# Kernel tuning notes

Measured on AMD Instinct MI355X. Metric: run time of the kernel, lower is better.

Reference implementation:

```python
import jax, jax.numpy as jnp
import numpy as np

B, D, H, W = 32, 256, 32, 32
K = 1024
COMMITMENT_COST = 0.25


def setup_inputs() -> dict:
    key = jax.random.key(0)
    k1, k2 = jax.random.split(key)
    z = jax.random.normal(k1, (B, D, H, W), dtype=jnp.float32)
    # torch init: uniform_(-1/K, 1/K)
    emb_weight = jax.random.uniform(k2, (K, D), dtype=jnp.float32,
                                    minval=-1.0 / K, maxval=1.0 / K)
    return {"z": z, "emb_weight": emb_weight}


def reference(z, emb_weight):
    b, c, h, w = z.shape
    # [B, D, H, W] -> [B*H*W, D]
    z_flat = jnp.transpose(z, (0, 2, 3, 1)).reshape(-1, c)
    # squared-distance: ||z||^2 + ||e||^2 - 2 z.e  -> [N, K]
    distances = (jnp.sum(z_flat ** 2, axis=1, keepdims=True)
                 + jnp.sum(emb_weight ** 2, axis=1)[None, :]
                 - 2.0 * jnp.matmul(z_flat, emb_weight.T))
    encoding_indices = jnp.argmin(distances, axis=1)  # [N]
    z_q = emb_weight[encoding_indices]                # [N, D]
    z_q = z_q.reshape(b, h, w, c).transpose(0, 3, 1, 2)  # [B, D, H, W]

    q_latent_loss = jnp.mean((jax.lax.stop_gradient(z_q) - z) ** 2)
    e_latent_loss = jnp.mean((z_q - jax.lax.stop_gradient(z)) ** 2)
    loss = q_latent_loss + COMMITMENT_COST * e_latent_loss

    # straight-through estimator
    z_q = z + jax.lax.stop_gradient(z_q - z)
    return z_q, loss, encoding_indices
```

## Files before the change

kernel.cpp:

```cpp
#include <hip/hip_runtime.h>

#define NPTS  32768
#define DIM   256
#define KCB   1024

#define ZQ_OFF   0
#define LOSS_OFF 8388608
#define IDX_OFF  8388609

typedef __attribute__((ext_vector_type(8))) short short8;
typedef __attribute__((ext_vector_type(4))) float f32x4;

__device__ __forceinline__ int z_base(int n) { return ((n >> 10) << 18) | (n & 1023); }

__device__ __forceinline__ unsigned short f2bf(float f) {
    unsigned u = __float_as_uint(f);
    u += 0x7FFFu + ((u >> 16) & 1u);
    return (unsigned short)(u >> 16);
}

__device__ __forceinline__ unsigned long long pack_vi(float v, int i) {
    unsigned int u = __float_as_uint(v);
    unsigned int key = (u & 0x80000000u) ? ~u : u;
    return ((unsigned long long)key << 32) | (unsigned int)i;
}

__device__ __forceinline__ float np_half_sq(const float* __restrict__ p, int stride) {
    float S[16];
#pragma unroll
    for (int l = 0; l < 16; ++l) {
        float t[8];
#pragma unroll
        for (int j = 0; j < 8; ++j) {
            float v = p[(j * 16 + l) * stride];
            t[j] = __fmul_rn(v, v);
        }
        S[l] = __fadd_rn(__fadd_rn(__fadd_rn(t[0], t[1]), __fadd_rn(t[2], t[3])),
                         __fadd_rn(__fadd_rn(t[4], t[5]), __fadd_rn(t[6], t[7])));
    }
    float u[8];
#pragma unroll
    for (int i = 0; i < 8; ++i) u[i] = __fadd_rn(S[i], S[i + 8]);
    float v4[4];
#pragma unroll
    for (int i = 0; i < 4; ++i) v4[i] = __fadd_rn(u[i], u[i + 4]);
    return __fadd_rn(__fadd_rn(v4[0], v4[2]), __fadd_rn(v4[1], v4[3]));
}
__device__ __forceinline__ float np_sum256_sq(const float* __restrict__ p, int stride) {
    return __fadd_rn(np_half_sq(p, stride), np_half_sq(p + 128 * stride, stride));
}

__global__ __launch_bounds__(256) void setup_kernel(
    const float* __restrict__ z, const float* __restrict__ emb,
    float* __restrict__ z2, float* __restrict__ eps,
    float* __restrict__ e2, float* __restrict__ e2h,
    unsigned short* __restrict__ ebf,
    double* __restrict__ loss_acc, unsigned int* __restrict__ ticket)
{
    if (blockIdx.x < 128) {
        int n = blockIdx.x * 256 + threadIdx.x;
        const float* p = z + z_base(n);
        z2[n] = np_sum256_sq(p, 1024);
        float a = 0.0f;
#pragma unroll 8
        for (int d = 0; d < 256; ++d) a += fabsf(p[d << 10]);
        eps[n] = __builtin_fmaf(1e-5f, a, 3e-4f);
        if (blockIdx.x == 0 && threadIdx.x == 0) { *loss_acc = 0.0; *ticket = 0u; }
    } else {
        int kb = (blockIdx.x - 128) * 256;
        for (int idx = threadIdx.x; idx < 256 * 256; idx += 256) {
            int k = kb + (idx >> 8), d = idx & 255;
            ebf[k * 256 + d] = f2bf(emb[k * 256 + d]);
        }
        int k = kb + threadIdx.x;
        float s = np_sum256_sq(emb + k * DIM, 1);
        e2[k] = s;
        e2h[k] = 0.5f * s;
    }
}

#define ZS_STRIDE 264
#define ES_STRIDE 40
#define ES_SIZE   (128 * ES_STRIDE)

__global__ __launch_bounds__(256) void dist_kernel(
    const float* __restrict__ z, const float* __restrict__ emb,
    const unsigned short* __restrict__ ebf,
    const float* __restrict__ z2w, const float* __restrict__ e2w,
    const float* __restrict__ e2hw, const float* __restrict__ epsw,
    float* __restrict__ out_idx)
{
    __shared__ __align__(16) short zs[64 * ZS_STRIDE];
    __shared__ __align__(16) short es[2 * ES_SIZE];
    __shared__ float redbuf[64 * 32];
    __shared__ int   cl[64 * 32];
    __shared__ float MxS[64], thrS[64], epsS[64], z2S[64];
    __shared__ unsigned int cntS[64];
    __shared__ unsigned long long bestS[64];
    __shared__ int ovfS;

    const int tid = threadIdx.x;
    const int w  = tid >> 6;
    const int l  = tid & 63;
    const int lq = l >> 4;
    const int lr = l & 15;
    const int n0 = blockIdx.x << 6;
    const int zb = z_base(n0);

    if (tid < 64) {
        MxS[tid] = -3.4e38f; thrS[tid] = 3.4e38f;
        cntS[tid] = 0u; bestS[tid] = 0x7FFFFFFFFFFFFFFFULL;
        epsS[tid] = epsw[n0 + tid]; z2S[tid] = z2w[n0 + tid];
    }
    if (tid == 0) ovfS = 0;
    for (int i = tid; i < 64 * 32; i += 256) cl[i] = 0;

    {
        int q = tid & 15, d0 = tid >> 4;
#pragma unroll 4
        for (int i = 0; i < 16; ++i) {
            int d = d0 + 16 * i;
            float4 v = *(const float4*)(z + zb + (d << 10) + 4 * q);
            zs[(4 * q + 0) * ZS_STRIDE + d] = (short)f2bf(v.x);
            zs[(4 * q + 1) * ZS_STRIDE + d] = (short)f2bf(v.y);
            zs[(4 * q + 2) * ZS_STRIDE + d] = (short)f2bf(v.z);
            zs[(4 * q + 3) * ZS_STRIDE + d] = (short)f2bf(v.w);
        }
    }

    const int skk = tid >> 1, sh = tid & 1;

    {
        const int4* src = (const int4*)(ebf + skk * 256 + sh * 16);
        int4 a = src[0], b = src[1];
        int4* dst = (int4*)(es + skk * ES_STRIDE + sh * 16);
        dst[0] = a; dst[1] = b;
    }
    __syncthreads();

    f32x4 acc[2][4];
#pragma unroll
    for (int mt = 0; mt < 2; ++mt)
#pragma unroll
        for (int nt = 0; nt < 4; ++nt) acc[mt][nt] = (f32x4)0.0f;

    const int mrow = 32 * (w & 1);
    const int kwv  = 64 * (w >> 1);

    int4 pa, pb;
#pragma unroll 1
    for (int g = 0; g < 72; ++g) {
        const int kt = g >> 3, dt = g & 7;
        const int k0 = (kt < 8 ? kt : 0) * 128;
        if (g < 71) {
            int gn = g + 1;
            int k0n = ((gn >> 3) < 8 ? (gn >> 3) : 0) * 128;
            const int4* src = (const int4*)(ebf + (k0n + skk) * 256 + (gn & 7) * 32 + sh * 16);
            pa = src[0]; pb = src[1];
        }
        {
            const short* esb = es + (g & 1) * ES_SIZE;
            const int dbase = dt * 32;
            short8 af0 = *(const short8*)(zs + (mrow + lr) * ZS_STRIDE + dbase + lq * 8);
            short8 af1 = *(const short8*)(zs + (mrow + 16 + lr) * ZS_STRIDE + dbase + lq * 8);
#pragma unroll
            for (int nt = 0; nt < 4; ++nt) {
                short8 bf = *(const short8*)(esb + (kwv + 16 * nt + lr) * ES_STRIDE + lq * 8);
                acc[0][nt] = __builtin_amdgcn_mfma_f32_16x16x32_bf16(af0, bf, acc[0][nt], 0, 0, 0);
                acc[1][nt] = __builtin_amdgcn_mfma_f32_16x16x32_bf16(af1, bf, acc[1][nt], 0, 0, 0);
            }
        }
        if (g < 71) {
            int4* dst = (int4*)(es + ((g + 1) & 1) * ES_SIZE + skk * ES_STRIDE + sh * 16);
            dst[0] = pa; dst[1] = pb;
            __syncthreads();
        }
        if (dt == 7) {
            if (g == 71) __syncthreads();
            float e2hr[4]; int kg[4];
#pragma unroll
            for (int nt = 0; nt < 4; ++nt) {
                kg[nt] = k0 + kwv + 16 * nt + lr;
                e2hr[nt] = e2hw[kg[nt]];
            }
            float vals[2][4][4];
#pragma unroll
            for (int mt = 0; mt < 2; ++mt)
#pragma unroll
                for (int nt = 0; nt < 4; ++nt)
#pragma unroll
                    for (int r = 0; r < 4; ++r)
                        vals[mt][nt][r] = acc[mt][nt][r] - e2hr[nt];
            if (kt < 8) {
#pragma unroll
                for (int mt = 0; mt < 2; ++mt)
#pragma unroll
                    for (int r = 0; r < 4; ++r) {
                        float m = fmaxf(fmaxf(vals[mt][0][r], vals[mt][1][r]),
                                        fmaxf(vals[mt][2][r], vals[mt][3][r]));
                        int row = mrow + 16 * mt + lq * 4 + r;
                        redbuf[row * 32 + (w >> 1) * 16 + lr] = m;
                    }
                __syncthreads();
                if (tid < 64) {
                    float m = redbuf[tid * 32];
#pragma unroll 8
                    for (int c = 1; c < 32; ++c) m = fmaxf(m, redbuf[tid * 32 + c]);
                    float Mx = fmaxf(MxS[tid], m);
                    MxS[tid] = Mx;
                    thrS[tid] = Mx - epsS[tid];
                }
                __syncthreads();
            }
            if (kt >= 1) {
#pragma unroll
                for (int mt = 0; mt < 2; ++mt)
#pragma unroll
                    for (int r = 0; r < 4; ++r) {
                        int row = mrow + 16 * mt + lq * 4 + r;
                        float th = thrS[row];
#pragma unroll
                        for (int nt = 0; nt < 4; ++nt) {
                            if (vals[mt][nt][r] >= th) {
                                unsigned int p = atomicAdd(&cntS[row], 1u);
                                if (p < 32u) cl[row * 32 + p] = kg[nt];
                                else atomicMax(&ovfS, 1);
                            }
                        }
                    }
            }
            if (kt < 8) {
#pragma unroll
                for (int mt = 0; mt < 2; ++mt)
#pragma unroll
                    for (int nt = 0; nt < 4; ++nt) acc[mt][nt] = (f32x4)0.0f;
            }
        }
    }

    __syncthreads();
    float* zx = (float*)es;
    const int pt = tid & 63;
    const int s0 = tid >> 6;
    unsigned int nc = cntS[pt]; if (nc > 32u) nc = 32u;
    bool  act[8]; int kE[8]; float accE[8];
#pragma unroll
    for (int j = 0; j < 8; ++j) {
        unsigned int s = (unsigned int)s0 + 4u * j;
        act[j] = s < nc;
        kE[j] = act[j] ? cl[pt * 32 + s] : 0;
        accE[j] = 0.0f;
    }
#pragma unroll 1
    for (int dt = 0; dt < 8; ++dt) {
        const int dbase = dt * 32;
        __syncthreads();
        {
            int q = tid & 15, dd0 = tid >> 4;
            float4 v0 = *(const float4*)(z + zb + ((dbase + dd0) << 10) + 4 * q);
            float4 v1 = *(const float4*)(z + zb + ((dbase + dd0 + 16) << 10) + 4 * q);
            *(float4*)(zx + dd0 * 68 + 4 * q) = v0;
            *(float4*)(zx + (dd0 + 16) * 68 + 4 * q) = v1;
        }
        __syncthreads();
#pragma unroll
        for (int j = 0; j < 8; ++j) {
            if (!act[j]) continue;
            const float* er = emb + kE[j] * 256 + dbase;
            float ev[32];
#pragma unroll
            for (int c = 0; c < 8; ++c) *(float4*)(ev + 4 * c) = *(const float4*)(er + 4 * c);
            float a = accE[j];
#pragma unroll
            for (int dd = 0; dd < 32; ++dd)
                a = __builtin_fmaf(zx[dd * 68 + pt], ev[dd], a);
            accE[j] = a;
        }
    }
#pragma unroll
    for (int j = 0; j < 8; ++j) {
        if (!act[j]) continue;
        int k = kE[j];
        float t1 = __fadd_rn(z2S[pt], e2w[k]);
        float d  = __fsub_rn(t1, __fmul_rn(2.0f, accE[j]));
        atomicMin(&bestS[pt], pack_vi(d, k));
    }
    __syncthreads();

    if (ovfS) {
        for (int row = 0; row < 64; ++row) {
            if (cntS[row] <= 32u) continue;
            float fa[4] = {0.f, 0.f, 0.f, 0.f};
            for (int dt = 0; dt < 8; ++dt) {
                const int dbase = dt * 32;
                __syncthreads();
                {
                    int q = tid & 15, dd0 = tid >> 4;
                    float4 v0 = *(const float4*)(z + zb + ((dbase + dd0) << 10) + 4 * q);
                    float4 v1 = *(const float4*)(z + zb + ((dbase + dd0 + 16) << 10) + 4 * q);
                    *(float4*)(zx + dd0 * 68 + 4 * q) = v0;
                    *(float4*)(zx + (dd0 + 16) * 68 + 4 * q) = v1;
                }
                __syncthreads();
                for (int c = 0; c < 4; ++c) {
                    const float* er = emb + (tid + 256 * c) * 256 + dbase;
                    for (int dd = 0; dd < 32; ++dd)
                        fa[c] = __builtin_fmaf(zx[dd * 68 + row], er[dd], fa[c]);
                }
            }
            for (int c = 0; c < 4; ++c) {
                int k = tid + 256 * c;
                float t1 = __fadd_rn(z2S[row], e2w[k]);
                float d  = __fsub_rn(t1, __fmul_rn(2.0f, fa[c]));
                atomicMin(&bestS[row], pack_vi(d, k));
            }
            __syncthreads();
        }
    }

    if (tid < 64)
        out_idx[n0 + tid] = (float)(unsigned int)(bestS[tid] & 0xFFFFFFFFULL);
}

__global__ __launch_bounds__(256) void zq_loss_kernel(
    const float* __restrict__ z, const float* __restrict__ emb,
    const float* __restrict__ idxv, float* __restrict__ zq,
    double* __restrict__ loss_acc, unsigned int* __restrict__ ticket,
    float* __restrict__ out_loss)
{
    const int n = blockIdx.x * 256 + threadIdx.x;
    const int kk = (int)idxv[n];
    const float* er = emb + kk * DIM;
    const int zb = z_base(n);
    double s = 0.0;
#pragma unroll 8
    for (int d = 0; d < DIM; ++d) {
        float ev = er[d];
        float zv = z[zb + (d << 10)];
        zq[zb + (d << 10)] = ev;
        float df = ev - zv;
        s = fma((double)df, (double)df, s);
    }
    for (int off = 32; off; off >>= 1) s += __shfl_down(s, off, 64);
    __shared__ double sred[4];
    if ((threadIdx.x & 63) == 0) sred[threadIdx.x >> 6] = s;
    __syncthreads();
    if (threadIdx.x == 0) {
        atomicAdd(loss_acc, (sred[0] + sred[1]) + (sred[2] + sred[3]));
        __threadfence();
        unsigned int old = atomicAdd(ticket, 1u);
        if (old == gridDim.x - 1) {
            double total = atomicAdd(loss_acc, 0.0);
            out_loss[0] = (float)(1.25 * (total / 8388608.0));
        }
    }
}

extern "C" void kernel_launch(void* const* d_in, const int* in_sizes, int n_in,
                              void* d_out, int out_size, void* d_ws, size_t ws_size,
                              hipStream_t stream) {
    const float* z   = (const float*)d_in[0];
    const float* emb = (const float*)d_in[1];
    float* out = (float*)d_out;

    float* z2w = (float*)d_ws;
    float* epsw = (float*)((char*)d_ws + 131072);
    float* e2w = (float*)((char*)d_ws + 262144);
    float* e2hw = (float*)((char*)d_ws + 266240);
    unsigned short* ebf = (unsigned short*)((char*)d_ws + 270336);
    double* loss_acc = (double*)((char*)d_ws + 794624);
    unsigned int* ticket = (unsigned int*)((char*)d_ws + 794632);

    setup_kernel<<<132, 256, 0, stream>>>(z, emb, z2w, epsw, e2w, e2hw, ebf,
                                          loss_acc, ticket);
    dist_kernel<<<NPTS / 64, 256, 0, stream>>>(z, emb, ebf, z2w, e2w, e2hw, epsw,
                                               out + IDX_OFF);
    zq_loss_kernel<<<NPTS / 256, 256, 0, stream>>>(z, emb, out + IDX_OFF,
                                                   out + ZQ_OFF, loss_acc, ticket,
                                                   out + LOSS_OFF);
}
```

Baseline: 250.2 us.

## Fuse zq/loss into distance kernel and stream codebook directly from global memory

The distance kernel is restructured so each wave owns a 256-entry slice of the codebook across all 64 points. It loads bf16 codebook fragments straight from global memory into registers and drops the LDS double buffer and the per-chunk block-wide syncs. Row maxima are reduced with cross-lane shuffles per wave instead of a shared redbuf and two barriers, and the candidate list grows to 48 slots. The zq gather and loss accumulation are fused into the tail of the same kernel, which removes the third launch, and setup fuses the abs-sum pass and vectorises the bf16 conversion. The risks are more global traffic for codebook fragments, more registers, and a per-wave running max that may be looser and admit more candidates.

Result: slower. 263.9 us (+5.5%).

```diff
diff --git a/kernel.cpp b/kernel.cpp
--- a/kernel.cpp
+++ b/kernel.cpp
@@ -44,6 +44,30 @@
     float v4[4];
 #pragma unroll
     for (int i = 0; i < 4; ++i) v4[i] = __fadd_rn(u[i], u[i + 4]);
+    return __fadd_rn(__fadd_rn(v4[0], v4[2]), __fadd_rn(v4[1], v4[3]));
+}
+__device__ __forceinline__ float np_half_sq_abs(const float* __restrict__ p, int stride,
+                                                float* asum) {
+    float S[16]; float a = *asum;
+#pragma unroll
+    for (int l = 0; l < 16; ++l) {
+        float t[8];
+#pragma unroll
+        for (int j = 0; j < 8; ++j) {
+            float v = p[(j * 16 + l) * stride];
+            t[j] = __fmul_rn(v, v);
+            a += fabsf(v);
+        }
+        S[l] = __fadd_rn(__fadd_rn(__fadd_rn(t[0], t[1]), __fadd_rn(t[2], t[3])),
+                         __fadd_rn(__fadd_rn(t[4], t[5]), __fadd_rn(t[6], t[7])));
+    }
+    float u[8];
+#pragma unroll
+    for (int i = 0; i < 8; ++i) u[i] = __fadd_rn(S[i], S[i + 8]);
+    float v4[4];
+#pragma unroll
+    for (int i = 0; i < 4; ++i) v4[i] = __fadd_rn(u[i], u[i + 4]);
+    *asum = a;
     return __fadd_rn(__fadd_rn(v4[0], v4[2]), __fadd_rn(v4[1], v4[3]));
 }
 __device__ __forceinline__ float np_sum256_sq(const float* __restrict__ p, int stride) {
@@ -60,17 +84,19 @@
     if (blockIdx.x < 128) {
         int n = blockIdx.x * 256 + threadIdx.x;
         const float* p = z + z_base(n);
-        z2[n] = np_sum256_sq(p, 1024);
         float a = 0.0f;
-#pragma unroll 8
-        for (int d = 0; d < 256; ++d) a += fabsf(p[d << 10]);
+        float h0 = np_half_sq_abs(p, 1024, &a);
+        float h1 = np_half_sq_abs(p + 128 * 1024, 1024, &a);
+        z2[n] = __fadd_rn(h0, h1);
         eps[n] = __builtin_fmaf(1e-5f, a, 3e-4f);
         if (blockIdx.x == 0 && threadIdx.x == 0) { *loss_acc = 0.0; *ticket = 0u; }
     } else {
         int kb = (blockIdx.x - 128) * 256;
-        for (int idx = threadIdx.x; idx < 256 * 256; idx += 256) {
-            int k = kb + (idx >> 8), d = idx & 255;
-            ebf[k * 256 + d] = f2bf(emb[k * 256 + d]);
+        const float2* s2 = (const float2*)(emb + kb * 256);
+        unsigned int* d2 = (unsigned int*)(ebf + kb * 256);
+        for (int i = threadIdx.x; i < 256 * 128; i += 256) {
+            float2 v = s2[i];
+            d2[i] = (unsigned)f2bf(v.x) | ((unsigned)f2bf(v.y) << 16);
         }
         int k = kb + threadIdx.x;
         float s = np_sum256_sq(emb + k * DIM, 1);
@@ -80,175 +106,158 @@
 }
 
 #define ZS_STRIDE 264
-#define ES_STRIDE 40
-#define ES_SIZE   (128 * ES_STRIDE)
-
-__global__ __launch_bounds__(256) void dist_kernel(
+#define CL_SLOTS  48
+
+__global__ __launch_bounds__(256) void dist_fused_kernel(
     const float* __restrict__ z, const float* __restrict__ emb,
     const unsigned short* __restrict__ ebf,
     const float* __restrict__ z2w, const float* __restrict__ e2w,
     const float* __restrict__ e2hw, const float* __restrict__ epsw,
-    float* __restrict__ out_idx)
+    float* __restrict__ out_idx, float* __restrict__ zq,
+    double* __restrict__ loss_acc, unsigned int* __restrict__ ticket,
+    float* __restrict__ out_loss)
 {
     __shared__ __align__(16) short zs[64 * ZS_STRIDE];
-    __shared__ __align__(16) short es[2 * ES_SIZE];
-    __shared__ float redbuf[64 * 32];
-    __shared__ int   cl[64 * 32];
-    __shared__ float MxS[64], thrS[64], epsS[64], z2S[64];
+    __shared__ int clS[64 * CL_SLOTS];
     __shared__ unsigned int cntS[64];
     __shared__ unsigned long long bestS[64];
+    __shared__ float z2S[64];
+    __shared__ double sredL[4];
     __shared__ int ovfS;
 
     const int tid = threadIdx.x;
-    const int w  = tid >> 6;
-    const int l  = tid & 63;
-    const int lq = l >> 4;
-    const int lr = l & 15;
-    const int n0 = blockIdx.x << 6;
-    const int zb = z_base(n0);
+    const int w   = tid >> 6;
+    const int l   = tid & 63;
+    const int n16 = l & 15;
+    const int q   = l >> 4;
+    const int n0  = blockIdx.x << 6;
+    const int zb  = z_base(n0);
+    const int kq  = w << 8;
 
     if (tid < 64) {
-        MxS[tid] = -3.4e38f; thrS[tid] = 3.4e38f;
-        cntS[tid] = 0u; bestS[tid] = 0x7FFFFFFFFFFFFFFFULL;
-        epsS[tid] = epsw[n0 + tid]; z2S[tid] = z2w[n0 + tid];
+        cntS[tid] = 0u;
+        bestS[tid] = 0x7FFFFFFFFFFFFFFFULL;
+        z2S[tid] = z2w[n0 + tid];
     }
     if (tid == 0) ovfS = 0;
-    for (int i = tid; i < 64 * 32; i += 256) cl[i] = 0;
 
     {
-        int q = tid & 15, d0 = tid >> 4;
+        int qq = tid & 15, d0 = tid >> 4;
 #pragma unroll 4
         for (int i = 0; i < 16; ++i) {
             int d = d0 + 16 * i;
-            float4 v = *(const float4*)(z + zb + (d << 10) + 4 * q);
-            zs[(4 * q + 0) * ZS_STRIDE + d] = (short)f2bf(v.x);
-            zs[(4 * q + 1) * ZS_STRIDE + d] = (short)f2bf(v.y);
-            zs[(4 * q + 2) * ZS_STRIDE + d] = (short)f2bf(v.z);
-            zs[(4 * q + 3) * ZS_STRIDE + d] = (short)f2bf(v.w);
-        }
-    }
-
-    const int skk = tid >> 1, sh = tid & 1;
-
-    {
-        const int4* src = (const int4*)(ebf + skk * 256 + sh * 16);
-        int4 a = src[0], b = src[1];
-        int4* dst = (int4*)(es + skk * ES_STRIDE + sh * 16);
-        dst[0] = a; dst[1] = b;
-    }
-    __syncthreads();
-
-    f32x4 acc[2][4];
-#pragma unroll
-    for (int mt = 0; mt < 2; ++mt)
+            float4 v = *(const float4*)(z + zb + (d << 10) + 4 * qq);
+            zs[(4 * qq + 0) * ZS_STRIDE + d] = (short)f2bf(v.x);
+            zs[(4 * qq + 1) * ZS_STRIDE + d] = (short)f2bf(v.y);
+            zs[(4 * qq + 2) * ZS_STRIDE + d] = (short)f2bf(v.z);
+            zs[(4 * qq + 3) * ZS_STRIDE + d] = (short)f2bf(v.w);
+        }
+    }
+
+    float epsr[4][4];
+#pragma unroll
+    for (int mt = 0; mt < 4; ++mt)
+#pragma unroll
+        for (int r = 0; r < 4; ++r)
+            epsr[mt][r] = epsw[n0 + mt * 16 + q * 4 + r];
+
+    __syncthreads();
+
+    f32x4 acc[4][4];
+    float Mx[4][4];
+#pragma unroll
+    for (int mt = 0; mt < 4; ++mt)
 #pragma unroll
         for (int nt = 0; nt < 4; ++nt) acc[mt][nt] = (f32x4)0.0f;
-
-    const int mrow = 32 * (w & 1);
-    const int kwv  = 64 * (w >> 1);
-
-    int4 pa, pb;
+#pragma unroll
+    for (int mt = 0; mt < 4; ++mt)
+#pragma unroll
+        for (int r = 0; r < 4; ++r) Mx[mt][r] = -3.4e38f;
+
+    int4 bcur[4];
+#pragma unroll
+    for (int nt = 0; nt < 4; ++nt)
+        bcur[nt] = *(const int4*)(ebf + ((kq + nt * 16 + n16) << 8) + q * 8);
+
 #pragma unroll 1
-    for (int g = 0; g < 72; ++g) {
-        const int kt = g >> 3, dt = g & 7;
-        const int k0 = (kt < 8 ? kt : 0) * 128;
-        if (g < 71) {
-            int gn = g + 1;
-            int k0n = ((gn >> 3) < 8 ? (gn >> 3) : 0) * 128;
-            const int4* src = (const int4*)(ebf + (k0n + skk) * 256 + (gn & 7) * 32 + sh * 16);
-            pa = src[0]; pb = src[1];
-        }
-        {
-            const short* esb = es + (g & 1) * ES_SIZE;
-            const int dbase = dt * 32;
-            short8 af0 = *(const short8*)(zs + (mrow + lr) * ZS_STRIDE + dbase + lq * 8);
-            short8 af1 = *(const short8*)(zs + (mrow + 16 + lr) * ZS_STRIDE + dbase + lq * 8);
+    for (int step = 0; step < 32; ++step) {
+        const int s = step >> 3, dc = step & 7;
+        short8 af[4];
+#pragma unroll
+        for (int mt = 0; mt < 4; ++mt)
+            af[mt] = *(const short8*)(zs + (mt * 16 + n16) * ZS_STRIDE + dc * 32 + q * 8);
+#pragma unroll
+        for (int nt = 0; nt < 4; ++nt) {
+            short8 bf = *(short8*)&bcur[nt];
+#pragma unroll
+            for (int mt = 0; mt < 4; ++mt)
+                acc[mt][nt] = __builtin_amdgcn_mfma_f32_16x16x32_bf16(af[mt], bf, acc[mt][nt], 0, 0, 0);
+        }
+        if (step < 31) {
+            const int sn = (step + 1) >> 3, dcn = (step + 1) & 7;
+#pragma unroll
+            for (int nt = 0; nt < 4; ++nt)
+                bcur[nt] = *(const int4*)(ebf + ((kq + sn * 64 + nt * 16 + n16) << 8) + dcn * 32 + q * 8);
+        }
+        if (dc == 7) {
+            float e2hr[4]; int kg[4];
 #pragma unroll
             for (int nt = 0; nt < 4; ++nt) {
-                short8 bf = *(const short8*)(esb + (kwv + 16 * nt + lr) * ES_STRIDE + lq * 8);
-                acc[0][nt] = __builtin_amdgcn_mfma_f32_16x16x32_bf16(af0, bf, acc[0][nt], 0, 0, 0);
-                acc[1][nt] = __builtin_amdgcn_mfma_f32_16x16x32_bf16(af1, bf, acc[1][nt], 0, 0, 0);
-            }
-        }
-        if (g < 71) {
-            int4* dst = (int4*)(es + ((g + 1) & 1) * ES_SIZE + skk * ES_STRIDE + sh * 16);
-            dst[0] = pa; dst[1] = pb;
-            __syncthreads();
-        }
-        if (dt == 7) {
-            if (g == 71) __syncthreads();
-            float e2hr[4]; int kg[4];
-#pragma unroll
-            for (int nt = 0; nt < 4; ++nt) {
-                kg[nt] = k0 + kwv + 16 * nt + lr;
+                kg[nt] = kq + s * 64 + nt * 16 + n16;
                 e2hr[nt] = e2hw[kg[nt]];
             }
-            float vals[2][4][4];
-#pragma unroll
-            for (int mt = 0; mt < 2; ++mt)
+#pragma unroll
+            for (int mt = 0; mt < 4; ++mt)
 #pragma unroll
                 for (int nt = 0; nt < 4; ++nt)
 #pragma unroll
                     for (int r = 0; r < 4; ++r)
-                        vals[mt][nt][r] = acc[mt][nt][r] - e2hr[nt];
-            if (kt < 8) {
-#pragma unroll
-                for (int mt = 0; mt < 2; ++mt)
-#pragma unroll
-                    for (int r = 0; r < 4; ++r) {
-                        float m = fmaxf(fmaxf(vals[mt][0][r], vals[mt][1][r]),
-                                        fmaxf(vals[mt][2][r], vals[mt][3][r]));
-                        int row = mrow + 16 * mt + lq * 4 + r;
-                        redbuf[row * 32 + (w >> 1) * 16 + lr] = m;
-                    }
-                __syncthreads();
-                if (tid < 64) {
-                    float m = redbuf[tid * 32];
-#pragma unroll 8
-                    for (int c = 1; c < 32; ++c) m = fmaxf(m, redbuf[tid * 32 + c]);
-                    float Mx = fmaxf(MxS[tid], m);
-                    MxS[tid] = Mx;
-                    thrS[tid] = Mx - epsS[tid];
+                        acc[mt][nt][r] -= e2hr[nt];
+#pragma unroll
+            for (int mt = 0; mt < 4; ++mt)
+#pragma unroll
+                for (int r = 0; r < 4; ++r) {
+                    float m = fmaxf(fmaxf(acc[mt][0][r], acc[mt][1][r]),
+                                    fmaxf(acc[mt][2][r], acc[mt][3][r]));
+                    m = fmaxf(m, __shfl_xor(m, 1, 64));
+                    m = fmaxf(m, __shfl_xor(m, 2, 64));
+                    m = fmaxf(m, __shfl_xor(m, 4, 64));
+                    m = fmaxf(m, __shfl_xor(m, 8, 64));
+                    Mx[mt][r] = fmaxf(Mx[mt][r], m);
                 }
-                __syncthreads();
-            }
-            if (kt >= 1) {
-#pragma unroll
-                for (int mt = 0; mt < 2; ++mt)
-#pragma unroll
-                    for (int r = 0; r < 4; ++r) {
-                        int row = mrow + 16 * mt + lq * 4 + r;
-                        float th = thrS[row];
-#pragma unroll
-                        for (int nt = 0; nt < 4; ++nt) {
-                            if (vals[mt][nt][r] >= th) {
-                                unsigned int p = atomicAdd(&cntS[row], 1u);
-                                if (p < 32u) cl[row * 32 + p] = kg[nt];
-                                else atomicMax(&ovfS, 1);
-                            }
+#pragma unroll
+            for (int mt = 0; mt < 4; ++mt)
+#pragma unroll
+                for (int r = 0; r < 4; ++r) {
+                    const float th = Mx[mt][r] - epsr[mt][r];
+                    const int row = mt * 16 + q * 4 + r;
+#pragma unroll
+                    for (int nt = 0; nt < 4; ++nt) {
+                        if (acc[mt][nt][r] >= th) {
+                            unsigned int p = atomicAdd(&cntS[row], 1u);
+                            if (p < CL_SLOTS) clS[row * CL_SLOTS + p] = kg[nt];
+                            else ovfS = 1;
                         }
                     }
-            }
-            if (kt < 8) {
-#pragma unroll
-                for (int mt = 0; mt < 2; ++mt)
-#pragma unroll
-                    for (int nt = 0; nt < 4; ++nt) acc[mt][nt] = (f32x4)0.0f;
-            }
-        }
-    }
-
-    __syncthreads();
-    float* zx = (float*)es;
+                }
+#pragma unroll
+            for (int mt = 0; mt < 4; ++mt)
+#pragma unroll
+                for (int nt = 0; nt < 4; ++nt) acc[mt][nt] = (f32x4)0.0f;
+        }
+    }
+
+    __syncthreads();
+    float* zx = (float*)zs;
     const int pt = tid & 63;
     const int s0 = tid >> 6;
-    unsigned int nc = cntS[pt]; if (nc > 32u) nc = 32u;
-    bool  act[8]; int kE[8]; float accE[8];
-#pragma unroll
-    for (int j = 0; j < 8; ++j) {
+    unsigned int nc = cntS[pt]; if (nc > CL_SLOTS) nc = CL_SLOTS;
+    bool  act[12]; int kE[12]; float accE[12];
+#pragma unroll
+    for (int j = 0; j < 12; ++j) {
         unsigned int s = (unsigned int)s0 + 4u * j;
         act[j] = s < nc;
-        kE[j] = act[j] ? cl[pt * 32 + s] : 0;
+        kE[j] = act[j] ? clS[pt * CL_SLOTS + s] : 0;
         accE[j] = 0.0f;
     }
 #pragma unroll 1
@@ -256,15 +265,15 @@
         const int dbase = dt * 32;
         __syncthreads();
         {
-            int q = tid & 15, dd0 = tid >> 4;
-            float4 v0 = *(const float4*)(z + zb + ((dbase + dd0) << 10) + 4 * q);
-            float4 v1 = *(const float4*)(z + zb + ((dbase + dd0 + 16) << 10) + 4 * q);
-            *(float4*)(zx + dd0 * 68 + 4 * q) = v0;
-            *(float4*)(zx + (dd0 + 16) * 68 + 4 * q) = v1;
+            int qq = tid & 15, dd0 = tid >> 4;
+            float4 v0 = *(const float4*)(z + zb + ((dbase + dd0) << 10) + 4 * qq);
+            float4 v1 = *(const float4*)(z + zb + ((dbase + dd0 + 16) << 10) + 4 * qq);
+            *(float4*)(zx + dd0 * 68 + 4 * qq) = v0;
+            *(float4*)(zx + (dd0 + 16) * 68 + 4 * qq) = v1;
         }
         __syncthreads();
 #pragma unroll
-        for (int j = 0; j < 8; ++j) {
+        for (int j = 0; j < 12; ++j) {
             if (!act[j]) continue;
             const float* er = emb + kE[j] * 256 + dbase;
             float ev[32];
@@ -278,7 +287,7 @@
         }
     }
 #pragma unroll
-    for (int j = 0; j < 8; ++j) {
+    for (int j = 0; j < 12; ++j) {
         if (!act[j]) continue;
         int k = kE[j];
         float t1 = __fadd_rn(z2S[pt], e2w[k]);
@@ -289,17 +298,17 @@
 
     if (ovfS) {
         for (int row = 0; row < 64; ++row) {
-            if (cntS[row] <= 32u) continue;
+            if (cntS[row] <= (unsigned)CL_SLOTS) continue;
             float fa[4] = {0.f, 0.f, 0.f, 0.f};
             for (int dt = 0; dt < 8; ++dt) {
                 const int dbase = dt * 32;
                 __syncthreads();
                 {
-                    int q = tid & 15, dd0 = tid >> 4;
-                    float4 v0 = *(const float4*)(z + zb + ((dbase + dd0) << 10) + 4 * q);
-                    float4 v1 = *(const float4*)(z + zb + ((dbase + dd0 + 16) << 10) + 4 * q);
-                    *(float4*)(zx + dd0 * 68 + 4 * q) = v0;
-                    *(float4*)(zx + (dd0 + 16) * 68 + 4 * q) = v1;
+                    int qq = tid & 15, dd0 = tid >> 4;
+                    float4 v0 = *(const float4*)(z + zb + ((dbase + dd0) << 10) + 4 * qq);
+                    float4 v1 = *(const float4*)(z + zb + ((dbase + dd0 + 16) << 10) + 4 * qq);
+                    *(float4*)(zx + dd0 * 68 + 4 * qq) = v0;
+                    *(float4*)(zx + (dd0 + 16) * 68 + 4 * qq) = v1;
                 }
                 __syncthreads();
                 for (int c = 0; c < 4; ++c) {
@@ -317,36 +326,34 @@
             __syncthreads();
         }
     }
+    __syncthreads();
 
     if (tid < 64)
         out_idx[n0 + tid] = (float)(unsigned int)(bestS[tid] & 0xFFFFFFFFULL);
-}
-
-__global__ __launch_bounds__(256) void zq_loss_kernel(
-    const float* __restrict__ z, const float* __restrict__ emb,
-    const float* __restrict__ idxv, float* __restrict__ zq,
-    double* __restrict__ loss_acc, unsigned int* __restrict__ ticket,
-    float* __restrict__ out_loss)
-{
-    const int n = blockIdx.x * 256 + threadIdx.x;
-    const int kk = (int)idxv[n];
-    const float* er = emb + kk * DIM;
-    const int zb = z_base(n);
-    double s = 0.0;
+
+    {
+        const int ptz = tid & 63;
+        const int dg  = tid >> 6;
+        const int kb  = (int)(unsigned int)(bestS[ptz] & 0xFFFFFFFFULL);
+        const float* er = emb + (kb << 8) + (dg << 6);
+        const float* zp = z  + zb + ((dg << 6) << 10) + ptz;
+        float*       qp = zq + zb + ((dg << 6) << 10) + ptz;
+        double sl = 0.0;
 #pragma unroll 8
-    for (int d = 0; d < DIM; ++d) {
-        float ev = er[d];
-        float zv = z[zb + (d << 10)];
-        zq[zb + (d << 10)] = ev;
-        float df = ev - zv;
-        s = fma((double)df, (double)df, s);
-    }
-    for (int off = 32; off; off >>= 1) s += __shfl_down(s, off, 64);
-    __shared__ double sred[4];
-    if ((threadIdx.x & 63) == 0) sred[threadIdx.x >> 6] = s;
-    __syncthreads();
-    if (threadIdx.x == 0) {
-        atomicAdd(loss_acc, (sred[0] + sred[1]) + (sred[2] + sred[3]));
+        for (int dd = 0; dd < 64; ++dd) {
+            float ev = er[dd];
+            float zv = zp[dd << 10];
+            qp[dd << 10] = ev;
+            float df = ev - zv;
+            sl = fma((double)df, (double)df, sl);
+        }
+        for (int off = 32; off; off >>= 1) sl += __shfl_down(sl, off, 64);
+        if (l == 0) sredL[w] = sl;
+    }
+    __syncthreads();
+    if (tid == 0) {
+        double t = (sredL[0] + sredL[1]) + (sredL[2] + sredL[3]);
+        atomicAdd(loss_acc, t);
         __threadfence();
         unsigned int old = atomicAdd(ticket, 1u);
         if (old == gridDim.x - 1) {
@@ -373,9 +380,7 @@
 
     setup_kernel<<<132, 256, 0, stream>>>(z, emb, z2w, epsw, e2w, e2hw, ebf,
                                           loss_acc, ticket);
-    dist_kernel<<<NPTS / 64, 256, 0, stream>>>(z, emb, ebf, z2w, e2w, e2hw, epsw,
-                                               out + IDX_OFF);
-    zq_loss_kernel<<<NPTS / 256, 256, 0, stream>>>(z, emb, out + IDX_OFF,
-                                                   out + ZQ_OFF, loss_acc, ticket,
-                                                   out + LOSS_OFF);
-}
+    dist_fused_kernel<<<NPTS / 64, 256, 0, stream>>>(z, emb, ebf, z2w, e2w, e2hw, epsw,
+                                                     out + IDX_OFF, out + ZQ_OFF,
+                                                     loss_acc, ticket, out + LOSS_OFF);
+}
```
